# Kernel tuning notes

Measured on AMD Instinct MI355X. Metric: run time of the kernel, lower is better.

## Reference

```python
import jax, jax.numpy as jnp
import numpy as np

G, D, H = 64, 16, 8   # n groups, per-group input dim, GRU hidden (feat_dim)
B, T = 64, 512


def setup_inputs() -> dict:
    key = jax.random.key(0)
    ks = jax.random.split(key, 5)
    s = 1.0 / np.sqrt(H)  # PyTorch GRU init: U(-1/sqrt(hidden), 1/sqrt(hidden))
    x = jax.random.normal(ks[0], (B, T, G * D), dtype=jnp.float32)
    W_ih = jax.random.uniform(ks[1], (G, 3 * H, D), jnp.float32, -s, s)
    W_hh = jax.random.uniform(ks[2], (G, 3 * H, H), jnp.float32, -s, s)
    b_ih = jax.random.uniform(ks[3], (G, 3 * H), jnp.float32, -s, s)
    b_hh = jax.random.uniform(ks[4], (G, 3 * H), jnp.float32, -s, s)
    return {"x": x, "W_ih": W_ih, "W_hh": W_hh, "b_ih": b_ih, "b_hh": b_hh}


def reference(x, W_ih, W_hh, b_ih, b_hh):
    # x: [B, T, G*D] -> per-group GRU, output [B, T, G, H]
    Bq, Tq, _ = x.shape
    xg = x.reshape(Bq, Tq, G, D)
    # Precompute all input-to-hidden gate projections as one grouped GEMM.
    gx = jnp.einsum('btgd,gkd->btgk', xg, W_ih) + b_ih  # [B, T, G, 3H]
    gx = jnp.moveaxis(gx, 1, 0)                          # [T, B, G, 3H]
    h0 = jnp.zeros((Bq, G, H), dtype=x.dtype)

    def step(h, gxt):
        gh = jnp.einsum('bgh,gkh->bgk', h, W_hh) + b_hh  # [B, G, 3H]
        xr, xz, xn = jnp.split(gxt, 3, axis=-1)          # PyTorch gate order: r, z, n
        hr, hz, hn = jnp.split(gh, 3, axis=-1)
        r = jax.nn.sigmoid(xr + hr)
        z = jax.nn.sigmoid(xz + hz)
        n = jnp.tanh(xn + r * hn)
        h_new = (1.0 - z) * n + z * h
        return h_new, h_new

    _, hs = jax.lax.scan(step, h0, gx)  # hs: [T, B, G, H]
    return jnp.moveaxis(hs, 0, 1)       # [B, T, G, H]
```

## Files before the change

### kernel.cpp

```cpp
#include <hip/hip_runtime.h>


#define Gn 64
#define Dn 16
#define Hn 8
#define Tn 512

typedef float v2f __attribute__((ext_vector_type(2)));

__device__ __forceinline__ float rcp_fast(float v) { return __builtin_amdgcn_rcpf(v); }
__device__ __forceinline__ float exp2_fast(float v) { return __builtin_amdgcn_exp2f(v); }

#define KNL (-1.44269504088896340736f)
#define KP2 ( 2.88539008177792681472f)

template <int CTRL>
__device__ __forceinline__ float dppf(float v) {
    return __int_as_float(
        __builtin_amdgcn_update_dpp(0, __float_as_int(v), CTRL, 0xF, 0xF, false));
}
template <int CTRL>
__device__ __forceinline__ v2f dpp2(v2f v) {
    v2f r;
    r.x = dppf<CTRL>(v.x);
    r.y = dppf<CTRL>(v.y);
    return r;
}

__global__ __attribute__((amdgpu_flat_work_group_size(64, 64),
                          amdgpu_waves_per_eu(1, 1)))
void mcgru_kernel(
    const float* __restrict__ x,
    const float* __restrict__ W_ih,
    const float* __restrict__ W_hh,
    const float* __restrict__ b_ih,
    const float* __restrict__ b_hh,
    float* __restrict__ out)
{
    const int tid  = blockIdx.x * blockDim.x + threadIdx.x;
    const int cell = tid >> 3;
    const int l    = tid & 7;
    const int g    = cell & (Gn - 1);
    const int b    = cell >> 6;
    const int s4   = l & 3;
    const int q    = l >> 2;

    int jmap[8];
#pragma unroll
    for (int k = 0; k < 8; ++k) {
        const int hi2 = k >> 2, r = k & 3;
        jmap[k] = ((q ^ hi2) << 2) | (s4 ^ r ^ (hi2 ? 3 : 0));
    }

    const float scale[3] = {KNL, KNL, KP2};

    v2f   wih[3][8];
    float whh[3][8];
    float bs[3];
    float bhn;
#pragma unroll
    for (int qg = 0; qg < 3; ++qg) {
        const int row = qg * Hn + l;
        const float sc = scale[qg];
        const float* wr = W_ih + ((size_t)g * 24 + row) * Dn;
#pragma unroll
        for (int k = 0; k < 8; ++k) {
            const int dp = jmap[k] * 2;
            wih[qg][k] = (v2f){wr[dp] * sc, wr[dp + 1] * sc};
        }
        const float* hrow = W_hh + ((size_t)g * 24 + row) * Hn;
#pragma unroll
        for (int k = 0; k < 8; ++k) whh[qg][k] = hrow[jmap[k]] * sc;
        if (qg < 2) {
            bs[qg] = (b_ih[g * 24 + row] + b_hh[g * 24 + row]) * sc;
        } else {
            bs[qg] = b_ih[g * 24 + row] * sc;
            bhn    = b_hh[g * 24 + row] * sc;
        }
    }
#pragma unroll
    for (int qg = 0; qg < 3; ++qg) {
#pragma unroll
        for (int i = 0; i < 8; ++i) asm volatile("" : "+v"(wih[qg][i]));
#pragma unroll
        for (int k = 0; k < 8; ++k) asm volatile("" : "+v"(whh[qg][k]));
        asm volatile("" : "+v"(bs[qg]));
    }
    asm volatile("" : "+v"(bhn));

    const float* xq = x   + ((size_t)b * Tn * Gn + g) * Dn + 2 * l;
    float*       op = out + ((size_t)b * Tn * Gn + g) * Hn + l;

    auto load_x = [&](int t) -> v2f {
        return *(const v2f*)(xq + (size_t)t * (Gn * Dn));
    };
    auto proj = [&](v2f xv, float* gx) {
        v2f X[8];
        X[0] = xv;
        X[1] = dpp2<0xB1>(xv);
        X[2] = dpp2<0x4E>(xv);
        X[3] = dpp2<0x1B>(xv);
        X[4] = dpp2<0x141>(X[0]);
        X[5] = dpp2<0x141>(X[1]);
        X[6] = dpp2<0x141>(X[2]);
        X[7] = dpp2<0x141>(X[3]);
#pragma unroll
        for (int qg = 0; qg < 3; ++qg) {
            v2f acc = wih[qg][0] * X[0];
#pragma unroll
            for (int i = 1; i < 8; ++i) acc += wih[qg][i] * X[i];
            gx[qg] = (bs[qg] + acc.x) + acc.y;
        }
    };

    float h = 0.0f;
    auto step = [&](const float* gx, int t) {
        float H[8];
        H[0] = h;
        H[1] = dppf<0xB1>(h);
        H[2] = dppf<0x4E>(h);
        H[3] = dppf<0x1B>(h);
        H[4] = dppf<0x141>(H[0]);
        H[5] = dppf<0x141>(H[1]);
        H[6] = dppf<0x141>(H[2]);
        H[7] = dppf<0x141>(H[3]);

        float gh[3];
#pragma unroll
        for (int qg = 0; qg < 3; ++qg) {
            float a = fmaf(whh[qg][1], H[1], whh[qg][0] * H[0]);
            a = fmaf(whh[qg][2], H[2], a);
            a = fmaf(whh[qg][3], H[3], a);
            float c = (qg == 2) ? fmaf(whh[qg][4], H[4], bhn)
                                : whh[qg][4] * H[4];
            c = fmaf(whh[qg][5], H[5], c);
            c = fmaf(whh[qg][6], H[6], c);
            c = fmaf(whh[qg][7], H[7], c);
            gh[qg] = a + c;
        }
        const float r  = rcp_fast(1.0f + exp2_fast(gx[0] + gh[0]));
        const float z  = rcp_fast(1.0f + exp2_fast(gx[1] + gh[1]));
        const float zh = z * h;
        const float om = 1.0f - z;
        const float e  = exp2_fast(fmaf(r, gh[2], gx[2]));
        const float n  = fmaf(-2.0f, rcp_fast(e + 1.0f), 1.0f);
        h = fmaf(n, om, zh);
        __builtin_nontemporal_store(h, op + (size_t)t * (Gn * Hn));
    };

    v2f   xr[8];
    float gx[4][3];

    {
        v2f t0 = load_x(0);
        v2f t1 = load_x(1);
        xr[2] = load_x(2); xr[3] = load_x(3); xr[4] = load_x(4);
        xr[5] = load_x(5); xr[6] = load_x(6); xr[7] = load_x(7);
        proj(t0, gx[0]);
        proj(t1, gx[1]);
    }

    for (int t = 0; t < Tn; t += 8) {
#pragma unroll
        for (int j = 0; j < 8; ++j) {
            const int s = t + j;
            int tl = s + 8; if (tl > Tn - 1) tl = Tn - 1;
            xr[j] = load_x(tl);
            asm volatile("" : "+v"(xr[(j + 2) & 7]));
            proj(xr[(j + 2) & 7], gx[(j + 2) & 3]);
            step(gx[j & 3], s);
        }
    }
}

extern "C" void kernel_launch(void* const* d_in, const int* in_sizes, int n_in,
                              void* d_out, int out_size, void* d_ws, size_t ws_size,
                              hipStream_t stream) {
    const float* x    = (const float*)d_in[0];
    const float* W_ih = (const float*)d_in[1];
    const float* W_hh = (const float*)d_in[2];
    const float* b_ih = (const float*)d_in[3];
    const float* b_hh = (const float*)d_in[4];
    float* out = (float*)d_out;

    dim3 grid(512), block(64);
    hipLaunchKernelGGL(mcgru_kernel, grid, block, 0, stream,
                       x, W_ih, W_hh, b_ih, b_hh, out);
}
```

Measured before the change: 289.2 us.

## Split each GRU cell across 16 lanes with half-dot products and DPP reduction

Each GRU cell now uses 16 lanes instead of 8. Each half of the lanes computes half of the input and hidden dot products, and a row-shift DPP add combines the two halves. The grid doubles to 1024 single-wave blocks. This halves the per-lane FMA chain on the serial recurrence, and the hidden-state matvec is issued before the next input projection so the two can overlap. In exchange there is an extra DPP reduction per gate, the activation math runs redundantly on both halves, and each wave covers fewer cells.

```diff
diff --git a/kernel.cpp b/kernel.cpp
--- a/kernel.cpp
+++ b/kernel.cpp
@@ -19,13 +19,6 @@
     return __int_as_float(
         __builtin_amdgcn_update_dpp(0, __float_as_int(v), CTRL, 0xF, 0xF, false));
 }
-template <int CTRL>
-__device__ __forceinline__ v2f dpp2(v2f v) {
-    v2f r;
-    r.x = dppf<CTRL>(v.x);
-    r.y = dppf<CTRL>(v.y);
-    return r;
-}
 
 __global__ __attribute__((amdgpu_flat_work_group_size(64, 64),
                           amdgpu_waves_per_eu(1, 1)))
@@ -37,107 +30,102 @@
     const float* __restrict__ b_hh,
     float* __restrict__ out)
 {
-    const int tid  = blockIdx.x * blockDim.x + threadIdx.x;
-    const int cell = tid >> 3;
-    const int l    = tid & 7;
-    const int g    = cell & (Gn - 1);
-    const int b    = cell >> 6;
-    const int s4   = l & 3;
-    const int q    = l >> 2;
+    const int lane  = threadIdx.x;
+    const int row16 = lane >> 4;
+    const int il    = lane & 15;
+    const int u     = il & 7;
+    const int p     = il >> 3;
+    const int cell  = blockIdx.x * 4 + row16;
+    const int g     = cell & (Gn - 1);
+    const int b     = cell >> 6;
 
-    int jmap[8];
-#pragma unroll
-    for (int k = 0; k < 8; ++k) {
-        const int hi2 = k >> 2, r = k & 3;
-        jmap[k] = ((q ^ hi2) << 2) | (s4 ^ r ^ (hi2 ? 3 : 0));
-    }
+    const int m[8] = {0, 1, 2, 3, 7, 6, 5, 4};
+    const int px   = p ? 7 : 0;
 
     const float scale[3] = {KNL, KNL, KP2};
 
-    v2f   wih[3][8];
-    float whh[3][8];
-    float bs[3];
-    float bhn;
+    v2f wihp[3][4];
+    v2f whhp[3][2];
+    v2f bsv[3];
+    v2f ghs;
 #pragma unroll
     for (int qg = 0; qg < 3; ++qg) {
-        const int row = qg * Hn + l;
+        const int row = qg * Hn + u;
         const float sc = scale[qg];
-        const float* wr = W_ih + ((size_t)g * 24 + row) * Dn;
+        const float* wr = W_ih + ((size_t)g * 24 + row) * Dn + 8 * p;
 #pragma unroll
-        for (int k = 0; k < 8; ++k) {
-            const int dp = jmap[k] * 2;
-            wih[qg][k] = (v2f){wr[dp] * sc, wr[dp + 1] * sc};
+        for (int j = 0; j < 4; ++j) {
+            wihp[qg][j] = (v2f){wr[u ^ m[2 * j]] * sc, wr[u ^ m[2 * j + 1]] * sc};
         }
-        const float* hrow = W_hh + ((size_t)g * 24 + row) * Hn;
+        const float* hr = W_hh + ((size_t)g * 24 + row) * Hn;
 #pragma unroll
-        for (int k = 0; k < 8; ++k) whh[qg][k] = hrow[jmap[k]] * sc;
-        if (qg < 2) {
-            bs[qg] = (b_ih[g * 24 + row] + b_hh[g * 24 + row]) * sc;
-        } else {
-            bs[qg] = b_ih[g * 24 + row] * sc;
-            bhn    = b_hh[g * 24 + row] * sc;
+        for (int j = 0; j < 2; ++j) {
+            whhp[qg][j] = (v2f){hr[u ^ ((2 * j) ^ px)] * sc,
+                                hr[u ^ ((2 * j + 1) ^ px)] * sc};
         }
+        float bias;
+        if (qg < 2) bias = (b_ih[g * 24 + row] + b_hh[g * 24 + row]) * sc;
+        else        bias = b_ih[g * 24 + row] * sc;
+        bsv[qg] = (p == 0) ? (v2f){bias, 0.0f} : (v2f){0.0f, 0.0f};
     }
+    ghs = (p == 0) ? (v2f){b_hh[g * 24 + 16 + u] * KP2, 0.0f}
+                   : (v2f){0.0f, 0.0f};
+
 #pragma unroll
     for (int qg = 0; qg < 3; ++qg) {
 #pragma unroll
-        for (int i = 0; i < 8; ++i) asm volatile("" : "+v"(wih[qg][i]));
+        for (int j = 0; j < 4; ++j) asm volatile("" : "+v"(wihp[qg][j]));
 #pragma unroll
-        for (int k = 0; k < 8; ++k) asm volatile("" : "+v"(whh[qg][k]));
-        asm volatile("" : "+v"(bs[qg]));
+        for (int j = 0; j < 2; ++j) asm volatile("" : "+v"(whhp[qg][j]));
+        asm volatile("" : "+v"(bsv[qg]));
     }
-    asm volatile("" : "+v"(bhn));
+    asm volatile("" : "+v"(ghs));
 
-    const float* xq = x   + ((size_t)b * Tn * Gn + g) * Dn + 2 * l;
-    float*       op = out + ((size_t)b * Tn * Gn + g) * Hn + l;
+    const float* xq = x   + ((size_t)b * Tn * (Gn * Dn)) + g * Dn + il;
+    float*       op = out + ((size_t)b * Tn * (Gn * Hn)) + g * Hn + u;
 
-    auto load_x = [&](int t) -> v2f {
-        return *(const v2f*)(xq + (size_t)t * (Gn * Dn));
-    };
-    auto proj = [&](v2f xv, float* gx) {
-        v2f X[8];
-        X[0] = xv;
-        X[1] = dpp2<0xB1>(xv);
-        X[2] = dpp2<0x4E>(xv);
-        X[3] = dpp2<0x1B>(xv);
-        X[4] = dpp2<0x141>(X[0]);
-        X[5] = dpp2<0x141>(X[1]);
-        X[6] = dpp2<0x141>(X[2]);
-        X[7] = dpp2<0x141>(X[3]);
+    auto load_x = [&](int t) -> float { return xq[(size_t)t * (Gn * Dn)]; };
+
+    auto proj = [&](float xv, float* gx) {
+        float X1 = dppf<0xB1>(xv);
+        float X2 = dppf<0x4E>(xv);
+        float X3 = dppf<0x1B>(xv);
+        v2f P0, P1, P2, P3;
+        P0.x = xv;              P0.y = X1;
+        P1.x = X2;              P1.y = X3;
+        P2.x = dppf<0x141>(xv); P2.y = dppf<0x141>(X1);
+        P3.x = dppf<0x141>(X2); P3.y = dppf<0x141>(X3);
 #pragma unroll
         for (int qg = 0; qg < 3; ++qg) {
-            v2f acc = wih[qg][0] * X[0];
-#pragma unroll
-            for (int i = 1; i < 8; ++i) acc += wih[qg][i] * X[i];
-            gx[qg] = (bs[qg] + acc.x) + acc.y;
+            v2f acc = wihp[qg][0] * P0 + bsv[qg];
+            acc = wihp[qg][1] * P1 + acc;
+            acc = wihp[qg][2] * P2 + acc;
+            acc = wihp[qg][3] * P3 + acc;
+            float part = acc.x + acc.y;
+            gx[qg] = dppf<0x128>(part) + part;
         }
     };
 
     float h = 0.0f;
-    auto step = [&](const float* gx, int t) {
-        float H[8];
-        H[0] = h;
-        H[1] = dppf<0xB1>(h);
-        H[2] = dppf<0x4E>(h);
-        H[3] = dppf<0x1B>(h);
-        H[4] = dppf<0x141>(H[0]);
-        H[5] = dppf<0x141>(H[1]);
-        H[6] = dppf<0x141>(H[2]);
-        H[7] = dppf<0x141>(H[3]);
-
-        float gh[3];
+    float gh[3];
+    auto step_head = [&]() {
+        const float M = dppf<0x141>(h);
+        const float B = p ? M : h;
+        v2f Hp0, Hp1;
+        Hp0.x = B;
+        Hp0.y = dppf<0xB1>(B);
+        Hp1.x = dppf<0x4E>(B);
+        Hp1.y = dppf<0x1B>(B);
 #pragma unroll
         for (int qg = 0; qg < 3; ++qg) {
-            float a = fmaf(whh[qg][1], H[1], whh[qg][0] * H[0]);
-            a = fmaf(whh[qg][2], H[2], a);
-            a = fmaf(whh[qg][3], H[3], a);
-            float c = (qg == 2) ? fmaf(whh[qg][4], H[4], bhn)
-                                : whh[qg][4] * H[4];
-            c = fmaf(whh[qg][5], H[5], c);
-            c = fmaf(whh[qg][6], H[6], c);
-            c = fmaf(whh[qg][7], H[7], c);
-            gh[qg] = a + c;
+            v2f acc = (qg == 2) ? (whhp[qg][0] * Hp0 + ghs)
+                                : (whhp[qg][0] * Hp0);
+            acc = whhp[qg][1] * Hp1 + acc;
+            float part = acc.x + acc.y;
+            gh[qg] = dppf<0x128>(part) + part;
         }
+    };
+    auto step_tail = [&](const float* gx, int t) {
         const float r  = rcp_fast(1.0f + exp2_fast(gx[0] + gh[0]));
         const float z  = rcp_fast(1.0f + exp2_fast(gx[1] + gh[1]));
         const float zh = z * h;
@@ -145,15 +133,15 @@
         const float e  = exp2_fast(fmaf(r, gh[2], gx[2]));
         const float n  = fmaf(-2.0f, rcp_fast(e + 1.0f), 1.0f);
         h = fmaf(n, om, zh);
-        __builtin_nontemporal_store(h, op + (size_t)t * (Gn * Hn));
+        if (p == 0)
+            __builtin_nontemporal_store(h, op + (size_t)t * (Gn * Hn));
     };
 
-    v2f   xr[8];
+    float xr[8];
     float gx[4][3];
-
     {
-        v2f t0 = load_x(0);
-        v2f t1 = load_x(1);
+        float t0 = load_x(0);
+        float t1 = load_x(1);
         xr[2] = load_x(2); xr[3] = load_x(3); xr[4] = load_x(4);
         xr[5] = load_x(5); xr[6] = load_x(6); xr[7] = load_x(7);
         proj(t0, gx[0]);
@@ -167,8 +155,9 @@
             int tl = s + 8; if (tl > Tn - 1) tl = Tn - 1;
             xr[j] = load_x(tl);
             asm volatile("" : "+v"(xr[(j + 2) & 7]));
+            step_head();
             proj(xr[(j + 2) & 7], gx[(j + 2) & 3]);
-            step(gx[j & 3], s);
+            step_tail(gx[j & 3], s);
         }
     }
 }
@@ -183,7 +172,7 @@
     const float* b_hh = (const float*)d_in[4];
     float* out = (float*)d_out;
 
-    dim3 grid(512), block(64);
+    dim3 grid(1024), block(64);
     hipLaunchKernelGGL(mcgru_kernel, grid, block, 0, stream,
                        x, W_ih, W_hh, b_ih, b_hh, out);
 }
```

Result: faster. 278.8 us (-3.6%).

## Warp-specialize input projection and recurrence with double-buffered LDS handoff

Applied to the files above, without the earlier changes.

Each block now has two waves. One wave loads x and computes the input-to-hidden gate projections into a double-buffered LDS chunk of 8 timesteps. The other wave runs the serial GRU recurrence, reading those gates from LDS, with barriers between chunks. This takes the projection FMAs and global loads off the recurrent critical path, at the cost of per-chunk barriers, LDS traffic and twice the threads per block.

```diff
diff --git a/kernel.cpp b/kernel.cpp
--- a/kernel.cpp
+++ b/kernel.cpp
@@ -5,6 +5,8 @@
 #define Dn 16
 #define Hn 8
 #define Tn 512
+#define CHUNK 8
+#define NCH (Tn / CHUNK)
 
 typedef float v2f __attribute__((ext_vector_type(2)));
 
@@ -27,7 +29,12 @@
     return r;
 }
 
-__global__ __attribute__((amdgpu_flat_work_group_size(64, 64),
+__device__ __forceinline__ void sync_lds() {
+    asm volatile("s_waitcnt lgkmcnt(0)" ::: "memory");
+    __builtin_amdgcn_s_barrier();
+}
+
+__global__ __attribute__((amdgpu_flat_work_group_size(128, 128),
                           amdgpu_waves_per_eu(1, 1)))
 void mcgru_kernel(
     const float* __restrict__ x,
@@ -37,13 +44,16 @@
     const float* __restrict__ b_hh,
     float* __restrict__ out)
 {
-    const int tid  = blockIdx.x * blockDim.x + threadIdx.x;
-    const int cell = tid >> 3;
-    const int l    = tid & 7;
-    const int g    = cell & (Gn - 1);
-    const int b    = cell >> 6;
-    const int s4   = l & 3;
-    const int q    = l >> 2;
+    __shared__ float gxs[2][CHUNK][3][64];
+
+    const int tlane = threadIdx.x & 63;
+    const int wid   = threadIdx.x >> 6;
+    const int c     = tlane >> 3;
+    const int u     = tlane & 7;
+    const int cell  = blockIdx.x * 8 + c;
+    const int g     = cell & (Gn - 1);
+    const int b     = cell >> 6;
+    const int s4 = u & 3, q = u >> 2;
 
     int jmap[8];
 #pragma unroll
@@ -51,124 +61,152 @@
         const int hi2 = k >> 2, r = k & 3;
         jmap[k] = ((q ^ hi2) << 2) | (s4 ^ r ^ (hi2 ? 3 : 0));
     }
-
     const float scale[3] = {KNL, KNL, KP2};
 
-    v2f   wih[3][8];
-    float whh[3][8];
-    float bs[3];
-    float bhn;
-#pragma unroll
-    for (int qg = 0; qg < 3; ++qg) {
-        const int row = qg * Hn + l;
-        const float sc = scale[qg];
-        const float* wr = W_ih + ((size_t)g * 24 + row) * Dn;
-#pragma unroll
-        for (int k = 0; k < 8; ++k) {
-            const int dp = jmap[k] * 2;
-            wih[qg][k] = (v2f){wr[dp] * sc, wr[dp + 1] * sc};
-        }
-        const float* hrow = W_hh + ((size_t)g * 24 + row) * Hn;
-#pragma unroll
-        for (int k = 0; k < 8; ++k) whh[qg][k] = hrow[jmap[k]] * sc;
-        if (qg < 2) {
-            bs[qg] = (b_ih[g * 24 + row] + b_hh[g * 24 + row]) * sc;
-        } else {
-            bs[qg] = b_ih[g * 24 + row] * sc;
-            bhn    = b_hh[g * 24 + row] * sc;
-        }
-    }
-#pragma unroll
-    for (int qg = 0; qg < 3; ++qg) {
-#pragma unroll
-        for (int i = 0; i < 8; ++i) asm volatile("" : "+v"(wih[qg][i]));
-#pragma unroll
-        for (int k = 0; k < 8; ++k) asm volatile("" : "+v"(whh[qg][k]));
-        asm volatile("" : "+v"(bs[qg]));
-    }
-    asm volatile("" : "+v"(bhn));
-
-    const float* xq = x   + ((size_t)b * Tn * Gn + g) * Dn + 2 * l;
-    float*       op = out + ((size_t)b * Tn * Gn + g) * Hn + l;
-
-    auto load_x = [&](int t) -> v2f {
-        return *(const v2f*)(xq + (size_t)t * (Gn * Dn));
-    };
-    auto proj = [&](v2f xv, float* gx) {
-        v2f X[8];
-        X[0] = xv;
-        X[1] = dpp2<0xB1>(xv);
-        X[2] = dpp2<0x4E>(xv);
-        X[3] = dpp2<0x1B>(xv);
-        X[4] = dpp2<0x141>(X[0]);
-        X[5] = dpp2<0x141>(X[1]);
-        X[6] = dpp2<0x141>(X[2]);
-        X[7] = dpp2<0x141>(X[3]);
+    if (wid == 1) {
+        v2f wih[3][8];
+        float bs[3];
 #pragma unroll
         for (int qg = 0; qg < 3; ++qg) {
-            v2f acc = wih[qg][0] * X[0];
-#pragma unroll
-            for (int i = 1; i < 8; ++i) acc += wih[qg][i] * X[i];
-            gx[qg] = (bs[qg] + acc.x) + acc.y;
-        }
-    };
-
-    float h = 0.0f;
-    auto step = [&](const float* gx, int t) {
-        float H[8];
-        H[0] = h;
-        H[1] = dppf<0xB1>(h);
-        H[2] = dppf<0x4E>(h);
-        H[3] = dppf<0x1B>(h);
-        H[4] = dppf<0x141>(H[0]);
-        H[5] = dppf<0x141>(H[1]);
-        H[6] = dppf<0x141>(H[2]);
-        H[7] = dppf<0x141>(H[3]);
-
-        float gh[3];
+            const int row = qg * Hn + u;
+            const float sc = scale[qg];
+            const float* wr = W_ih + ((size_t)g * 24 + row) * Dn;
+#pragma unroll
+            for (int k = 0; k < 8; ++k) {
+                const int dp = jmap[k] * 2;
+                wih[qg][k] = (v2f){wr[dp] * sc, wr[dp + 1] * sc};
+            }
+            bs[qg] = (qg < 2)
+                ? (b_ih[g * 24 + row] + b_hh[g * 24 + row]) * sc
+                : b_ih[g * 24 + row] * sc;
+        }
 #pragma unroll
         for (int qg = 0; qg < 3; ++qg) {
-            float a = fmaf(whh[qg][1], H[1], whh[qg][0] * H[0]);
-            a = fmaf(whh[qg][2], H[2], a);
-            a = fmaf(whh[qg][3], H[3], a);
-            float c = (qg == 2) ? fmaf(whh[qg][4], H[4], bhn)
-                                : whh[qg][4] * H[4];
-            c = fmaf(whh[qg][5], H[5], c);
-            c = fmaf(whh[qg][6], H[6], c);
-            c = fmaf(whh[qg][7], H[7], c);
-            gh[qg] = a + c;
-        }
-        const float r  = rcp_fast(1.0f + exp2_fast(gx[0] + gh[0]));
-        const float z  = rcp_fast(1.0f + exp2_fast(gx[1] + gh[1]));
-        const float zh = z * h;
-        const float om = 1.0f - z;
-        const float e  = exp2_fast(fmaf(r, gh[2], gx[2]));
-        const float n  = fmaf(-2.0f, rcp_fast(e + 1.0f), 1.0f);
-        h = fmaf(n, om, zh);
-        __builtin_nontemporal_store(h, op + (size_t)t * (Gn * Hn));
-    };
-
-    v2f   xr[8];
-    float gx[4][3];
-
-    {
-        v2f t0 = load_x(0);
-        v2f t1 = load_x(1);
-        xr[2] = load_x(2); xr[3] = load_x(3); xr[4] = load_x(4);
-        xr[5] = load_x(5); xr[6] = load_x(6); xr[7] = load_x(7);
-        proj(t0, gx[0]);
-        proj(t1, gx[1]);
-    }
-
-    for (int t = 0; t < Tn; t += 8) {
-#pragma unroll
-        for (int j = 0; j < 8; ++j) {
-            const int s = t + j;
-            int tl = s + 8; if (tl > Tn - 1) tl = Tn - 1;
-            xr[j] = load_x(tl);
-            asm volatile("" : "+v"(xr[(j + 2) & 7]));
-            proj(xr[(j + 2) & 7], gx[(j + 2) & 3]);
-            step(gx[j & 3], s);
+#pragma unroll
+            for (int i = 0; i < 8; ++i) asm volatile("" : "+v"(wih[qg][i]));
+            asm volatile("" : "+v"(bs[qg]));
+        }
+
+        const float* xq = x + ((size_t)b * Tn * Gn + g) * Dn + 2 * u;
+        auto load_x = [&](int t) -> v2f {
+            return *(const v2f*)(xq + (size_t)t * (Gn * Dn));
+        };
+        auto proj_store = [&](v2f xv, float* dst) {
+            v2f X[8];
+            X[0] = xv;
+            X[1] = dpp2<0xB1>(xv);
+            X[2] = dpp2<0x4E>(xv);
+            X[3] = dpp2<0x1B>(xv);
+            X[4] = dpp2<0x141>(X[0]);
+            X[5] = dpp2<0x141>(X[1]);
+            X[6] = dpp2<0x141>(X[2]);
+            X[7] = dpp2<0x141>(X[3]);
+#pragma unroll
+            for (int qg = 0; qg < 3; ++qg) {
+                v2f acc = wih[qg][0] * X[0];
+#pragma unroll
+                for (int i = 1; i < 8; ++i) acc += wih[qg][i] * X[i];
+                dst[qg * 64] = (bs[qg] + acc.x) + acc.y;
+            }
+        };
+
+        v2f xrA[CHUNK], xrB[CHUNK];
+#pragma unroll
+        for (int j = 0; j < CHUNK; ++j) xrA[j] = load_x(j);
+#pragma unroll
+        for (int j = 0; j < CHUNK; ++j) xrB[j] = load_x(CHUNK + j);
+#pragma unroll
+        for (int j = 0; j < CHUNK; ++j)
+            proj_store(xrA[j], &gxs[0][j][0][tlane]);
+        sync_lds();
+
+        for (int k = 0; k < NCH; k += 2) {
+            if (k + 1 < NCH) {
+#pragma unroll
+                for (int j = 0; j < CHUNK; ++j)
+                    proj_store(xrB[j], &gxs[1][j][0][tlane]);
+            }
+            if (k + 2 < NCH) {
+#pragma unroll
+                for (int j = 0; j < CHUNK; ++j)
+                    xrA[j] = load_x((k + 2) * CHUNK + j);
+            }
+            sync_lds();
+            if (k + 2 < NCH) {
+#pragma unroll
+                for (int j = 0; j < CHUNK; ++j)
+                    proj_store(xrA[j], &gxs[0][j][0][tlane]);
+            }
+            if (k + 3 < NCH) {
+#pragma unroll
+                for (int j = 0; j < CHUNK; ++j)
+                    xrB[j] = load_x((k + 3) * CHUNK + j);
+            }
+            sync_lds();
+        }
+    } else {
+        float whh[3][8], bhn;
+#pragma unroll
+        for (int qg = 0; qg < 3; ++qg) {
+            const int row = qg * Hn + u;
+            const float sc = scale[qg];
+            const float* hrow = W_hh + ((size_t)g * 24 + row) * Hn;
+#pragma unroll
+            for (int k = 0; k < 8; ++k) whh[qg][k] = hrow[jmap[k]] * sc;
+        }
+        bhn = b_hh[g * 24 + 2 * Hn + u] * KP2;
+#pragma unroll
+        for (int qg = 0; qg < 3; ++qg)
+#pragma unroll
+            for (int k = 0; k < 8; ++k) asm volatile("" : "+v"(whh[qg][k]));
+        asm volatile("" : "+v"(bhn));
+
+        float* op = out + ((size_t)b * Tn * Gn + g) * Hn + u;
+        float h = 0.0f;
+        sync_lds();
+
+        for (int k = 0; k < NCH; ++k) {
+            const float* bufp = &gxs[k & 1][0][0][tlane];
+#pragma unroll
+            for (int j = 0; j < CHUNK; ++j) {
+                const float gx0 = bufp[(j * 3 + 0) * 64];
+                const float gx1 = bufp[(j * 3 + 1) * 64];
+                const float gx2 = bufp[(j * 3 + 2) * 64];
+
+                float H[8];
+                H[0] = h;
+                H[1] = dppf<0xB1>(h);
+                H[2] = dppf<0x4E>(h);
+                H[3] = dppf<0x1B>(h);
+                H[4] = dppf<0x141>(H[0]);
+                H[5] = dppf<0x141>(H[1]);
+                H[6] = dppf<0x141>(H[2]);
+                H[7] = dppf<0x141>(H[3]);
+
+                float gh[3];
+#pragma unroll
+                for (int qg = 0; qg < 3; ++qg) {
+                    float a = fmaf(whh[qg][1], H[1], whh[qg][0] * H[0]);
+                    a = fmaf(whh[qg][2], H[2], a);
+                    a = fmaf(whh[qg][3], H[3], a);
+                    float cc = (qg == 2) ? fmaf(whh[qg][4], H[4], bhn)
+                                         : whh[qg][4] * H[4];
+                    cc = fmaf(whh[qg][5], H[5], cc);
+                    cc = fmaf(whh[qg][6], H[6], cc);
+                    cc = fmaf(whh[qg][7], H[7], cc);
+                    gh[qg] = a + cc;
+                }
+                const float r  = rcp_fast(1.0f + exp2_fast(gx0 + gh[0]));
+                const float z  = rcp_fast(1.0f + exp2_fast(gx1 + gh[1]));
+                const float zh = z * h;
+                const float om = 1.0f - z;
+                const float e  = exp2_fast(fmaf(r, gh[2], gx2));
+                const float n  = fmaf(-2.0f, rcp_fast(e + 1.0f), 1.0f);
+                h = fmaf(n, om, zh);
+                __builtin_nontemporal_store(
+                    h, op + (size_t)(k * CHUNK + j) * (Gn * Hn));
+            }
+            sync_lds();
         }
     }
 }
@@ -183,7 +221,7 @@
     const float* b_hh = (const float*)d_in[4];
     float* out = (float*)d_out;
 
-    dim3 grid(512), block(64);
+    dim3 grid(512), block(128);
     hipLaunchKernelGGL(mcgru_kernel, grid, block, 0, stream,
                        x, W_ih, W_hh, b_ih, b_hh, out);
 }
```

New measurement: 268.4 us. 7.2% less time.
